# Kernel optimization log

Measured on AMD Instinct MI355X. Metric: run time of the kernel, lower is better.

## Reference

```python
import jax, jax.numpy as jnp
import numpy as np

N_PTS = 2_000_000
RESO = 256          # per-axis resolution of the factorized planes
OUT_DIM = 3         # output_coordinate_dim
RANK = 4            # rank per plane component
FEAT_RESO = 64      # resolution of the final feature grid
FEAT_DIM = 32       # feature_dim
INIT_STD = 0.1


def grid_sample_2d(plane, coords):
    """Bilinear sample. plane: [C,H,W]; coords: [N,2] (x,y) in [-1,1].
    align_corners=True, border clamping. Returns [N,C]."""
    C, H, W = plane.shape
    x = jnp.clip((coords[:, 0] + 1.0) * 0.5 * (W - 1), 0.0, W - 1)
    y = jnp.clip((coords[:, 1] + 1.0) * 0.5 * (H - 1), 0.0, H - 1)
    x0 = jnp.clip(jnp.floor(x), 0, W - 2).astype(jnp.int32)
    y0 = jnp.clip(jnp.floor(y), 0, H - 2).astype(jnp.int32)
    wx = (x - x0)[None, :]
    wy = (y - y0)[None, :]
    v00 = plane[:, y0, x0]
    v01 = plane[:, y0, x0 + 1]
    v10 = plane[:, y0 + 1, x0]
    v11 = plane[:, y0 + 1, x0 + 1]
    out = (v00 * (1 - wx) * (1 - wy) + v01 * wx * (1 - wy)
           + v10 * (1 - wx) * wy + v11 * wx * wy)  # [C,N]
    return out.T


def grid_sample_3d(vol, coords):
    """Trilinear sample. vol: [C,D,H,W]; coords: [N,3] (x,y,z) in [-1,1]
    mapping to (W,H,D). align_corners=True, border clamping. Returns [N,C]."""
    C, D, H, W = vol.shape
    x = jnp.clip((coords[:, 0] + 1.0) * 0.5 * (W - 1), 0.0, W - 1)
    y = jnp.clip((coords[:, 1] + 1.0) * 0.5 * (H - 1), 0.0, H - 1)
    z = jnp.clip((coords[:, 2] + 1.0) * 0.5 * (D - 1), 0.0, D - 1)
    x0 = jnp.clip(jnp.floor(x), 0, W - 2).astype(jnp.int32)
    y0 = jnp.clip(jnp.floor(y), 0, H - 2).astype(jnp.int32)
    z0 = jnp.clip(jnp.floor(z), 0, D - 2).astype(jnp.int32)
    wx = (x - x0)[None, :]
    wy = (y - y0)[None, :]
    wz = (z - z0)[None, :]
    out = jnp.zeros((C, x.shape[0]), dtype=vol.dtype)
    for dz, fz in ((z0, 1 - wz), (z0 + 1, wz)):
        for dy, fy in ((y0, 1 - wy), (y0 + 1, wy)):
            for dx, fx in ((x0, 1 - wx), (x0 + 1, wx)):
                out = out + vol[:, dz, dy, dx] * (fz * fy * fx)
    return out.T


def setup_inputs() -> dict:
    key = jax.random.key(0)
    ks = jax.random.split(key, 5)
    pts = jax.random.uniform(ks[0], (N_PTS, 3), dtype=jnp.float32,
                             minval=-1.0, maxval=1.0)
    C = OUT_DIM * RANK
    plane01 = jax.random.normal(ks[1], (C, RESO, RESO), dtype=jnp.float32) * INIT_STD
    plane02 = jax.random.normal(ks[2], (C, RESO, RESO), dtype=jnp.float32) * INIT_STD
    plane12 = jax.random.normal(ks[3], (C, RESO, RESO), dtype=jnp.float32) * INIT_STD
    features = jax.random.normal(
        ks[4], (FEAT_DIM, FEAT_RESO, FEAT_RESO, FEAT_RESO), dtype=jnp.float32) * INIT_STD
    return {"pts": pts, "plane01": plane01, "plane02": plane02,
            "plane12": plane12, "features": features}


def reference(pts, plane01, plane02, plane12, features):
    # coo_combs = [(0,1),(0,2),(1,2)]; plane ci shaped [out_dim*rank, reso[c1], reso[c0]]
    n = pts.shape[0]
    interp = grid_sample_2d(plane01, pts[:, (0, 1)]).reshape(n, OUT_DIM, RANK)
    interp = interp * grid_sample_2d(plane02, pts[:, (0, 2)]).reshape(n, OUT_DIM, RANK)
    interp = interp * grid_sample_2d(plane12, pts[:, (1, 2)]).reshape(n, OUT_DIM, RANK)
    coords = interp.sum(axis=-1)  # [N, out_dim] -> new coordinates in [-1,1]-ish
    out = grid_sample_3d(features, coords)  # [N, feature_dim]
    return out
```

## Files before the change

kernel.cpp:

```cpp
#include <hip/hip_runtime.h>


constexpr int kNPts   = 2000000;
constexpr int kReso   = 256;
constexpr int kPix    = kReso * kReso;
constexpr int kCPlane = 12;
constexpr int kFReso  = 64;
constexpr int kNVox   = kFReso * kFReso * kFReso;
constexpr int kFDim   = 32;
constexpr int kCellRes = 16;
constexpr int kNCell  = kCellRes * kCellRes * kCellRes;
constexpr int kCap    = 640;
constexpr unsigned kOvCap = 2000000u;

constexpr int kThreads    = 256;
constexpr int kPtsPerScB  = 16384;
constexpr int kScBlocks   = (kNPts + kPtsPerScB - 1) / kPtsPerScB;
constexpr int kPlaneBlocks = (3 * (kPix / 4)) / kThreads;
constexpr int kFeatBlocks  = (kNVox / 4) / kThreads;
constexpr int kPrepBlocks  = kScBlocks + kPlaneBlocks + kFeatBlocks;
constexpr int kOvBlocks    = 16;

constexpr int kStage = 18;
constexpr int kRowF  = kStage * kCPlane;

static __device__ __forceinline__ float clampf(float v, float lo, float hi) {
  return fminf(fmaxf(v, lo), hi);
}

static __device__ __forceinline__ float4 f4_scale_add(float4 v, float s, float4 acc) {
  acc.x = fmaf(v.x, s, acc.x);
  acc.y = fmaf(v.y, s, acc.y);
  acc.z = fmaf(v.z, s, acc.z);
  acc.w = fmaf(v.w, s, acc.w);
  return acc;
}

static __device__ __forceinline__ int cell_of(float x, float y, float z) {
  int xq = min(kCellRes - 1, max(0, (int)((x + 1.0f) * (0.5f * kCellRes))));
  int yq = min(kCellRes - 1, max(0, (int)((y + 1.0f) * (0.5f * kCellRes))));
  int zq = min(kCellRes - 1, max(0, (int)((z + 1.0f) * (0.5f * kCellRes))));
  return (zq * kCellRes + yq) * kCellRes + xq;
}

static __device__ __forceinline__ void sample_plane_tr(
    const float* __restrict__ plane, float cx, float cy, float4 r[3]) {
  float x = clampf((cx + 1.0f) * 0.5f * (float)(kReso - 1), 0.0f, (float)(kReso - 1));
  float y = clampf((cy + 1.0f) * 0.5f * (float)(kReso - 1), 0.0f, (float)(kReso - 1));
  float fx0 = fminf(floorf(x), (float)(kReso - 2));
  float fy0 = fminf(floorf(y), (float)(kReso - 2));
  int x0 = (int)fx0;
  int y0 = (int)fy0;
  float wx = x - fx0;
  float wy = y - fy0;
  float w00 = (1.0f - wx) * (1.0f - wy);
  float w01 = wx * (1.0f - wy);
  float w10 = (1.0f - wx) * wy;
  float w11 = wx * wy;
  const float4* v00 = (const float4*)(plane + (size_t)(y0 * kReso + x0) * kCPlane);
  const float4* v01 = (const float4*)(plane + (size_t)(y0 * kReso + x0 + 1) * kCPlane);
  const float4* v10 = (const float4*)(plane + (size_t)((y0 + 1) * kReso + x0) * kCPlane);
  const float4* v11 = (const float4*)(plane + (size_t)((y0 + 1) * kReso + x0 + 1) * kCPlane);
#pragma unroll
  for (int i = 0; i < 3; ++i) {
    float4 acc = make_float4(0.f, 0.f, 0.f, 0.f);
    acc = f4_scale_add(v00[i], w00, acc);
    acc = f4_scale_add(v01[i], w01, acc);
    acc = f4_scale_add(v10[i], w10, acc);
    acc = f4_scale_add(v11[i], w11, acc);
    r[i] = acc;
  }
}

static __device__ __forceinline__ void bilin_lds(
    const float* __restrict__ sp, int lc, int lr, float wc, float wr, float4 r[3]) {
  const float* t00 = sp + (lr * kStage + lc) * kCPlane;
  const float* t01 = t00 + kCPlane;
  const float* t10 = t00 + kRowF;
  const float* t11 = t10 + kCPlane;
  float w00 = (1.0f - wc) * (1.0f - wr);
  float w01 = wc * (1.0f - wr);
  float w10 = (1.0f - wc) * wr;
  float w11 = wc * wr;
#pragma unroll
  for (int i = 0; i < 3; ++i) {
    float4 acc = make_float4(0.f, 0.f, 0.f, 0.f);
    acc = f4_scale_add(((const float4*)t00)[i], w00, acc);
    acc = f4_scale_add(((const float4*)t01)[i], w01, acc);
    acc = f4_scale_add(((const float4*)t10)[i], w10, acc);
    acc = f4_scale_add(((const float4*)t11)[i], w11, acc);
    r[i] = acc;
  }
}


__global__ __launch_bounds__(256) void prep_fused(
    const float* __restrict__ pts,
    const float* __restrict__ p0, const float* __restrict__ p1,
    const float* __restrict__ p2, const float* __restrict__ featSrc,
    float* __restrict__ planeT, float* __restrict__ featT,
    unsigned* __restrict__ counts, unsigned* __restrict__ ovcnt,
    unsigned* __restrict__ ovlist, unsigned* __restrict__ buckets) {
  __shared__ unsigned short s_cellid[kPtsPerScB];
  __shared__ unsigned s_hist[kNCell];
  __shared__ unsigned s_loc[kNCell];

  int b = blockIdx.x;
  int tid = threadIdx.x;

  if (b < kScBlocks) {
    for (int i = tid; i < kNCell; i += kThreads) s_hist[i] = 0u;
    __syncthreads();

    size_t base = (size_t)b * kPtsPerScB;
#pragma unroll 4
    for (int k = 0; k < kPtsPerScB / kThreads; ++k) {
      int sl = k * kThreads + tid;
      size_t g = base + sl;
      unsigned short cid = 0xFFFFu;
      if (g < (size_t)kNPts) {
        const float* pp = pts + 3 * g;
        cid = (unsigned short)cell_of(pp[0], pp[1], pp[2]);
        atomicAdd(&s_hist[cid], 1u);
      }
      s_cellid[sl] = cid;
    }
    __syncthreads();

    for (int c = tid; c < kNCell; c += kThreads) {
      unsigned h = s_hist[c];
      s_loc[c] = 0u;
      s_hist[c] = h ? atomicAdd(&counts[c], h) : 0u;
    }
    __syncthreads();

#pragma unroll 4
    for (int k = 0; k < kPtsPerScB / kThreads; ++k) {
      int sl = k * kThreads + tid;
      unsigned short cid = s_cellid[sl];
      if (cid == 0xFFFFu) continue;
      unsigned r = atomicAdd(&s_loc[cid], 1u);
      unsigned pos = s_hist[cid] + r;
      unsigned idx = (unsigned)(base + sl);
      if (pos < (unsigned)kCap) {
        buckets[(size_t)cid * kCap + pos] = idx;
      } else {
        unsigned op = atomicAdd(ovcnt, 1u);
        if (op < kOvCap) ovlist[op] = idx;
      }
    }
  } else if (b < kScBlocks + kPlaneBlocks) {
    int t = (b - kScBlocks) * kThreads + tid;
    constexpr int quarter = kPix / 4;
    int p = t / quarter;
    int pix4 = (t % quarter) * 4;
    const float* src = (p == 0) ? p0 : (p == 1) ? p1 : p2;
    float4 v[kCPlane];
#pragma unroll
    for (int c = 0; c < kCPlane; ++c)
      v[c] = *(const float4*)(src + (size_t)c * kPix + pix4);
    float* dstb = planeT + ((size_t)p * kPix + pix4) * kCPlane;
#pragma unroll
    for (int j = 0; j < 4; ++j) {
      float e[kCPlane];
#pragma unroll
      for (int c = 0; c < kCPlane; ++c) {
        const float* vc = (const float*)&v[c];
        e[c] = vc[j];
      }
      float4* dst = (float4*)(dstb + (size_t)j * kCPlane);
      dst[0] = make_float4(e[0], e[1], e[2], e[3]);
      dst[1] = make_float4(e[4], e[5], e[6], e[7]);
      dst[2] = make_float4(e[8], e[9], e[10], e[11]);
    }
  } else {
    int t = (b - kScBlocks - kPlaneBlocks) * kThreads + tid;
    int vox4 = t * 4;
#pragma unroll
    for (int chunk = 0; chunk < 4; ++chunk) {
      float4 v[8];
#pragma unroll
      for (int c8 = 0; c8 < 8; ++c8) {
        int c = chunk * 8 + c8;
        v[c8] = *(const float4*)(featSrc + (size_t)c * kNVox + vox4);
      }
#pragma unroll
      for (int j = 0; j < 4; ++j) {
        float e[8];
#pragma unroll
        for (int c8 = 0; c8 < 8; ++c8) e[c8] = ((const float*)&v[c8])[j];
        float4* dst = (float4*)(featT + (size_t)(vox4 + j) * kFDim + chunk * 8);
        dst[0] = make_float4(e[0], e[1], e[2], e[3]);
        dst[1] = make_float4(e[4], e[5], e[6], e[7]);
      }
    }
  }
}


__global__ __launch_bounds__(256) void lrh_cells(
    const float* __restrict__ pts, const float* __restrict__ planeT,
    const float* __restrict__ feat,
    const unsigned* __restrict__ counts, const unsigned* __restrict__ buckets,
    const unsigned* __restrict__ ovcnt, const unsigned* __restrict__ ovlist,
    float* __restrict__ out) {
  __shared__ float s_plane[3][kStage * kRowF];

  int b = blockIdx.x;
  int tid = threadIdx.x;

  if (b < kNCell) {
    int cellx = b & (kCellRes - 1);
    int celly = (b >> 4) & (kCellRes - 1);
    int cellz = b >> 8;
    int sx = min(cellx * 255 / 16, kReso - kStage);
    int sy = min(celly * 255 / 16, kReso - kStage);
    int sz = min(cellz * 255 / 16, kReso - kStage);
    const int colS[3] = {sx, sx, sy};
    const int rowS[3] = {sy, sz, sz};

#pragma unroll
    for (int p = 0; p < 3; ++p) {
      const float* src = planeT + (size_t)p * kPix * kCPlane;
      float* dst = s_plane[p];
      for (int i = tid; i < kStage * (kRowF / 4); i += kThreads) {
        int r = i / (kRowF / 4);
        int q = i - r * (kRowF / 4);
        float4 v = *(const float4*)(src +
            ((size_t)(rowS[p] + r) * kReso + colS[p]) * kCPlane + q * 4);
        *(float4*)(dst + r * kRowF + q * 4) = v;
      }
    }
    __syncthreads();

    unsigned craw = counts[b];
    int cnt = craw < (unsigned)kCap ? (int)craw : kCap;

    for (int base = 0; base < cnt; base += kThreads) {
      int slot = base + tid;
      if (slot >= cnt) break;
      int n = (int)buckets[(size_t)b * kCap + slot];

      const float* pp = pts + 3 * (size_t)n;
      float xx = pp[0], yy = pp[1], zz = pp[2];

      float px = clampf((xx + 1.0f) * 0.5f * (float)(kReso - 1), 0.0f, (float)(kReso - 1));
      float py = clampf((yy + 1.0f) * 0.5f * (float)(kReso - 1), 0.0f, (float)(kReso - 1));
      float pz = clampf((zz + 1.0f) * 0.5f * (float)(kReso - 1), 0.0f, (float)(kReso - 1));
      float fx0 = fminf(floorf(px), (float)(kReso - 2));
      float fy0 = fminf(floorf(py), (float)(kReso - 2));
      float fz0 = fminf(floorf(pz), (float)(kReso - 2));
      float wx = px - fx0, wy = py - fy0, wz = pz - fz0;
      int lx = min(max((int)fx0 - sx, 0), kStage - 2);
      int ly = min(max((int)fy0 - sy, 0), kStage - 2);
      int lz = min(max((int)fz0 - sz, 0), kStage - 2);

      float4 a[3], bb[3], c3[3];
      bilin_lds(s_plane[0], lx, ly, wx, wy, a);
      bilin_lds(s_plane[1], lx, lz, wx, wz, bb);
      bilin_lds(s_plane[2], ly, lz, wy, wz, c3);

      float coord[3];
#pragma unroll
      for (int d = 0; d < 3; ++d) {
        float mx = a[d].x * bb[d].x * c3[d].x;
        float my = a[d].y * bb[d].y * c3[d].y;
        float mz = a[d].z * bb[d].z * c3[d].z;
        float mw = a[d].w * bb[d].w * c3[d].w;
        coord[d] = (mx + my) + (mz + mw);
      }

      float gx = clampf((coord[0] + 1.0f) * 0.5f * (float)(kFReso - 1), 0.0f, (float)(kFReso - 1));
      float gy = clampf((coord[1] + 1.0f) * 0.5f * (float)(kFReso - 1), 0.0f, (float)(kFReso - 1));
      float gz = clampf((coord[2] + 1.0f) * 0.5f * (float)(kFReso - 1), 0.0f, (float)(kFReso - 1));
      float gfx0 = fminf(floorf(gx), (float)(kFReso - 2));
      float gfy0 = fminf(floorf(gy), (float)(kFReso - 2));
      float gfz0 = fminf(floorf(gz), (float)(kFReso - 2));
      int ix0 = (int)gfx0;
      int iy0 = (int)gfy0;
      int iz0 = (int)gfz0;
      float fwx = gx - gfx0, fwy = gy - gfy0, fwz = gz - gfz0;

      float acc[kFDim];
#pragma unroll
      for (int c = 0; c < kFDim; ++c) acc[c] = 0.0f;

#pragma unroll
      for (int dz = 0; dz < 2; ++dz) {
        float fzw = dz ? fwz : (1.0f - fwz);
#pragma unroll
        for (int dy = 0; dy < 2; ++dy) {
          float fyw = dy ? fwy : (1.0f - fwy);
#pragma unroll
          for (int dx = 0; dx < 2; ++dx) {
            float w = fzw * fyw * (dx ? fwx : (1.0f - fwx));
            int vox = ((iz0 + dz) * kFReso + (iy0 + dy)) * kFReso + (ix0 + dx);
            const float4* v = (const float4*)(feat + (size_t)vox * kFDim);
#pragma unroll
            for (int k = 0; k < 8; ++k) {
              float4 t = v[k];
              acc[4 * k + 0] = fmaf(t.x, w, acc[4 * k + 0]);
              acc[4 * k + 1] = fmaf(t.y, w, acc[4 * k + 1]);
              acc[4 * k + 2] = fmaf(t.z, w, acc[4 * k + 2]);
              acc[4 * k + 3] = fmaf(t.w, w, acc[4 * k + 3]);
            }
          }
        }
      }

      float4* o = (float4*)(out + (size_t)n * kFDim);
#pragma unroll
      for (int k = 0; k < 8; ++k)
        o[k] = make_float4(acc[4 * k], acc[4 * k + 1], acc[4 * k + 2], acc[4 * k + 3]);
    }
  } else {
    unsigned ov = *ovcnt;
    if (ov > kOvCap) ov = kOvCap;
    const float* p01 = planeT;
    const float* p02 = planeT + (size_t)kPix * kCPlane;
    const float* p12 = planeT + (size_t)2 * kPix * kCPlane;
    for (unsigned i = (unsigned)(b - kNCell) * kThreads + tid; i < ov;
         i += (unsigned)kOvBlocks * kThreads) {
      int n = (int)ovlist[i];
      float cx = pts[3 * (size_t)n + 0];
      float cy = pts[3 * (size_t)n + 1];
      float cz = pts[3 * (size_t)n + 2];

      float4 a[3], bb[3], c3[3];
      sample_plane_tr(p01, cx, cy, a);
      sample_plane_tr(p02, cx, cz, bb);
      sample_plane_tr(p12, cy, cz, c3);

      float coord[3];
#pragma unroll
      for (int d = 0; d < 3; ++d) {
        float mx = a[d].x * bb[d].x * c3[d].x;
        float my = a[d].y * bb[d].y * c3[d].y;
        float mz = a[d].z * bb[d].z * c3[d].z;
        float mw = a[d].w * bb[d].w * c3[d].w;
        coord[d] = (mx + my) + (mz + mw);
      }

      float gx = clampf((coord[0] + 1.0f) * 0.5f * (float)(kFReso - 1), 0.0f, (float)(kFReso - 1));
      float gy = clampf((coord[1] + 1.0f) * 0.5f * (float)(kFReso - 1), 0.0f, (float)(kFReso - 1));
      float gz = clampf((coord[2] + 1.0f) * 0.5f * (float)(kFReso - 1), 0.0f, (float)(kFReso - 1));
      float fx0 = fminf(floorf(gx), (float)(kFReso - 2));
      float fy0 = fminf(floorf(gy), (float)(kFReso - 2));
      float fz0 = fminf(floorf(gz), (float)(kFReso - 2));
      int ix0 = (int)fx0;
      int iy0 = (int)fy0;
      int iz0 = (int)fz0;
      float wx = gx - fx0, wy = gy - fy0, wz = gz - fz0;

      float acc[kFDim];
#pragma unroll
      for (int c = 0; c < kFDim; ++c) acc[c] = 0.0f;
#pragma unroll
      for (int dz = 0; dz < 2; ++dz) {
        float fzw = dz ? wz : (1.0f - wz);
#pragma unroll
        for (int dy = 0; dy < 2; ++dy) {
          float fyw = dy ? wy : (1.0f - wy);
#pragma unroll
          for (int dx = 0; dx < 2; ++dx) {
            float w = fzw * fyw * (dx ? wx : (1.0f - wx));
            int vox = ((iz0 + dz) * kFReso + (iy0 + dy)) * kFReso + (ix0 + dx);
            const float4* v = (const float4*)(feat + (size_t)vox * kFDim);
#pragma unroll
            for (int k = 0; k < 8; ++k) {
              float4 t = v[k];
              acc[4 * k + 0] = fmaf(t.x, w, acc[4 * k + 0]);
              acc[4 * k + 1] = fmaf(t.y, w, acc[4 * k + 1]);
              acc[4 * k + 2] = fmaf(t.z, w, acc[4 * k + 2]);
              acc[4 * k + 3] = fmaf(t.w, w, acc[4 * k + 3]);
            }
          }
        }
      }
      float4* o = (float4*)(out + (size_t)n * kFDim);
#pragma unroll
      for (int k = 0; k < 8; ++k)
        o[k] = make_float4(acc[4 * k], acc[4 * k + 1], acc[4 * k + 2], acc[4 * k + 3]);
    }
  }
}

extern "C" void kernel_launch(void* const* d_in, const int* in_sizes, int n_in,
                              void* d_out, int out_size, void* d_ws, size_t ws_size,
                              hipStream_t stream) {
  const float* pts  = (const float*)d_in[0];
  const float* p01  = (const float*)d_in[1];
  const float* p02  = (const float*)d_in[2];
  const float* p12  = (const float*)d_in[3];
  const float* feat = (const float*)d_in[4];
  float* out = (float*)d_out;

  const size_t off_planeT  = 0;
  const size_t sz_planeT   = (size_t)3 * kPix * kCPlane * sizeof(float);
  const size_t off_featT   = off_planeT + sz_planeT;
  const size_t sz_featT    = (size_t)kNVox * kFDim * sizeof(float);
  const size_t off_counts  = off_featT + sz_featT;
  const size_t sz_counts   = (size_t)kNCell * sizeof(unsigned);
  const size_t off_ovcnt   = off_counts + sz_counts;
  const size_t sz_ovcnt    = 256;
  const size_t off_ovlist  = off_ovcnt + sz_ovcnt;
  const size_t sz_ovlist   = (size_t)kOvCap * sizeof(unsigned);
  const size_t off_buckets = off_ovlist + sz_ovlist;
  const size_t sz_buckets  = (size_t)kNCell * kCap * sizeof(unsigned);
  const size_t need = off_buckets + sz_buckets;

  if (ws_size < need) return;

  char* wsb = (char*)d_ws;
  float*    planeT  = (float*)(wsb + off_planeT);
  float*    featT   = (float*)(wsb + off_featT);
  unsigned* counts  = (unsigned*)(wsb + off_counts);
  unsigned* ovcnt   = (unsigned*)(wsb + off_ovcnt);
  unsigned* ovlist  = (unsigned*)(wsb + off_ovlist);
  unsigned* buckets = (unsigned*)(wsb + off_buckets);

  hipMemsetAsync(counts, 0, sz_counts + sz_ovcnt, stream);
  hipLaunchKernelGGL(prep_fused, dim3(kPrepBlocks), dim3(kThreads), 0, stream,
                     pts, p01, p02, p12, feat, planeT, featT,
                     counts, ovcnt, ovlist, buckets);
  hipLaunchKernelGGL(lrh_cells, dim3(kNCell + kOvBlocks), dim3(kThreads), 0, stream,
                     pts, planeT, featT, counts, buckets, ovcnt, ovlist, out);
}
```

Baseline: 526.3 us.

## Split trilinear feature gather across 8 lanes per point and widen prep blocks

```diff
diff --git a/kernel.cpp b/kernel.cpp
--- a/kernel.cpp
+++ b/kernel.cpp
@@ -13,11 +13,12 @@
 constexpr int kCap    = 640;
 constexpr unsigned kOvCap = 2000000u;
 
-constexpr int kThreads    = 256;
-constexpr int kPtsPerScB  = 16384;
-constexpr int kScBlocks   = (kNPts + kPtsPerScB - 1) / kPtsPerScB;
-constexpr int kPlaneBlocks = (3 * (kPix / 4)) / kThreads;
-constexpr int kFeatBlocks  = (kNVox / 4) / kThreads;
+constexpr int kThreads     = 256;
+constexpr int kPrepThreads = 1024;
+constexpr int kPtsPerScB   = 16384;
+constexpr int kScBlocks    = (kNPts + kPtsPerScB - 1) / kPtsPerScB;
+constexpr int kPlaneBlocks = (3 * (kPix / 4)) / kPrepThreads;
+constexpr int kFeatBlocks  = (kNVox / 4) / kPrepThreads;
 constexpr int kPrepBlocks  = kScBlocks + kPlaneBlocks + kFeatBlocks;
 constexpr int kOvBlocks    = 16;
 
@@ -94,7 +95,7 @@
 }
 
 
-__global__ __launch_bounds__(256) void prep_fused(
+__global__ __launch_bounds__(1024) void prep_fused(
     const float* __restrict__ pts,
     const float* __restrict__ p0, const float* __restrict__ p1,
     const float* __restrict__ p2, const float* __restrict__ featSrc,
@@ -109,13 +110,12 @@
   int tid = threadIdx.x;
 
   if (b < kScBlocks) {
-    for (int i = tid; i < kNCell; i += kThreads) s_hist[i] = 0u;
+    for (int i = tid; i < kNCell; i += kPrepThreads) s_hist[i] = 0u;
     __syncthreads();
 
     size_t base = (size_t)b * kPtsPerScB;
-#pragma unroll 4
-    for (int k = 0; k < kPtsPerScB / kThreads; ++k) {
-      int sl = k * kThreads + tid;
+    for (int k = 0; k < kPtsPerScB / kPrepThreads; ++k) {
+      int sl = k * kPrepThreads + tid;
       size_t g = base + sl;
       unsigned short cid = 0xFFFFu;
       if (g < (size_t)kNPts) {
@@ -127,16 +127,15 @@
     }
     __syncthreads();
 
-    for (int c = tid; c < kNCell; c += kThreads) {
+    for (int c = tid; c < kNCell; c += kPrepThreads) {
       unsigned h = s_hist[c];
       s_loc[c] = 0u;
       s_hist[c] = h ? atomicAdd(&counts[c], h) : 0u;
     }
     __syncthreads();
 
-#pragma unroll 4
-    for (int k = 0; k < kPtsPerScB / kThreads; ++k) {
-      int sl = k * kThreads + tid;
+    for (int k = 0; k < kPtsPerScB / kPrepThreads; ++k) {
+      int sl = k * kPrepThreads + tid;
       unsigned short cid = s_cellid[sl];
       if (cid == 0xFFFFu) continue;
       unsigned r = atomicAdd(&s_loc[cid], 1u);
@@ -150,7 +149,7 @@
       }
     }
   } else if (b < kScBlocks + kPlaneBlocks) {
-    int t = (b - kScBlocks) * kThreads + tid;
+    int t = (b - kScBlocks) * kPrepThreads + tid;
     constexpr int quarter = kPix / 4;
     int p = t / quarter;
     int pix4 = (t % quarter) * 4;
@@ -174,7 +173,7 @@
       dst[2] = make_float4(e[8], e[9], e[10], e[11]);
     }
   } else {
-    int t = (b - kScBlocks - kPlaneBlocks) * kThreads + tid;
+    int t = (b - kScBlocks - kPlaneBlocks) * kPrepThreads + tid;
     int vox4 = t * 4;
 #pragma unroll
     for (int chunk = 0; chunk < 4; ++chunk) {
@@ -205,6 +204,11 @@
     const unsigned* __restrict__ ovcnt, const unsigned* __restrict__ ovlist,
     float* __restrict__ out) {
   __shared__ float s_plane[3][kStage * kRowF];
+  __shared__ int   s_n[kThreads];
+  __shared__ int   s_vox[kThreads];
+  __shared__ float s_wx[kThreads];
+  __shared__ float s_wy[kThreads];
+  __shared__ float s_wz[kThreads];
 
   int b = blockIdx.x;
   int tid = threadIdx.x;
@@ -238,80 +242,100 @@
 
     for (int base = 0; base < cnt; base += kThreads) {
       int slot = base + tid;
-      if (slot >= cnt) break;
-      int n = (int)buckets[(size_t)b * kCap + slot];
-
-      const float* pp = pts + 3 * (size_t)n;
-      float xx = pp[0], yy = pp[1], zz = pp[2];
-
-      float px = clampf((xx + 1.0f) * 0.5f * (float)(kReso - 1), 0.0f, (float)(kReso - 1));
-      float py = clampf((yy + 1.0f) * 0.5f * (float)(kReso - 1), 0.0f, (float)(kReso - 1));
-      float pz = clampf((zz + 1.0f) * 0.5f * (float)(kReso - 1), 0.0f, (float)(kReso - 1));
-      float fx0 = fminf(floorf(px), (float)(kReso - 2));
-      float fy0 = fminf(floorf(py), (float)(kReso - 2));
-      float fz0 = fminf(floorf(pz), (float)(kReso - 2));
-      float wx = px - fx0, wy = py - fy0, wz = pz - fz0;
-      int lx = min(max((int)fx0 - sx, 0), kStage - 2);
-      int ly = min(max((int)fy0 - sy, 0), kStage - 2);
-      int lz = min(max((int)fz0 - sz, 0), kStage - 2);
-
-      float4 a[3], bb[3], c3[3];
-      bilin_lds(s_plane[0], lx, ly, wx, wy, a);
-      bilin_lds(s_plane[1], lx, lz, wx, wz, bb);
-      bilin_lds(s_plane[2], ly, lz, wy, wz, c3);
-
-      float coord[3];
-#pragma unroll
-      for (int d = 0; d < 3; ++d) {
-        float mx = a[d].x * bb[d].x * c3[d].x;
-        float my = a[d].y * bb[d].y * c3[d].y;
-        float mz = a[d].z * bb[d].z * c3[d].z;
-        float mw = a[d].w * bb[d].w * c3[d].w;
-        coord[d] = (mx + my) + (mz + mw);
-      }
-
-      float gx = clampf((coord[0] + 1.0f) * 0.5f * (float)(kFReso - 1), 0.0f, (float)(kFReso - 1));
-      float gy = clampf((coord[1] + 1.0f) * 0.5f * (float)(kFReso - 1), 0.0f, (float)(kFReso - 1));
-      float gz = clampf((coord[2] + 1.0f) * 0.5f * (float)(kFReso - 1), 0.0f, (float)(kFReso - 1));
-      float gfx0 = fminf(floorf(gx), (float)(kFReso - 2));
-      float gfy0 = fminf(floorf(gy), (float)(kFReso - 2));
-      float gfz0 = fminf(floorf(gz), (float)(kFReso - 2));
-      int ix0 = (int)gfx0;
-      int iy0 = (int)gfy0;
-      int iz0 = (int)gfz0;
-      float fwx = gx - gfx0, fwy = gy - gfy0, fwz = gz - gfz0;
-
-      float acc[kFDim];
-#pragma unroll
-      for (int c = 0; c < kFDim; ++c) acc[c] = 0.0f;
-
-#pragma unroll
-      for (int dz = 0; dz < 2; ++dz) {
-        float fzw = dz ? fwz : (1.0f - fwz);
-#pragma unroll
-        for (int dy = 0; dy < 2; ++dy) {
-          float fyw = dy ? fwy : (1.0f - fwy);
-#pragma unroll
-          for (int dx = 0; dx < 2; ++dx) {
-            float w = fzw * fyw * (dx ? fwx : (1.0f - fwx));
-            int vox = ((iz0 + dz) * kFReso + (iy0 + dy)) * kFReso + (ix0 + dx);
-            const float4* v = (const float4*)(feat + (size_t)vox * kFDim);
-#pragma unroll
-            for (int k = 0; k < 8; ++k) {
-              float4 t = v[k];
-              acc[4 * k + 0] = fmaf(t.x, w, acc[4 * k + 0]);
-              acc[4 * k + 1] = fmaf(t.y, w, acc[4 * k + 1]);
-              acc[4 * k + 2] = fmaf(t.z, w, acc[4 * k + 2]);
-              acc[4 * k + 3] = fmaf(t.w, w, acc[4 * k + 3]);
-            }
-          }
+      int n = -1;
+      int ivox = 0;
+      float wxo = 0.f, wyo = 0.f, wzo = 0.f;
+      if (slot < cnt) {
+        n = (int)buckets[(size_t)b * kCap + slot];
+        const float* pp = pts + 3 * (size_t)n;
+        float xx = pp[0], yy = pp[1], zz = pp[2];
+
+        float px = clampf((xx + 1.0f) * 0.5f * (float)(kReso - 1), 0.0f, (float)(kReso - 1));
+        float py = clampf((yy + 1.0f) * 0.5f * (float)(kReso - 1), 0.0f, (float)(kReso - 1));
+        float pz = clampf((zz + 1.0f) * 0.5f * (float)(kReso - 1), 0.0f, (float)(kReso - 1));
+        float fx0 = fminf(floorf(px), (float)(kReso - 2));
+        float fy0 = fminf(floorf(py), (float)(kReso - 2));
+        float fz0 = fminf(floorf(pz), (float)(kReso - 2));
+        float wx = px - fx0, wy = py - fy0, wz = pz - fz0;
+        int lx = min(max((int)fx0 - sx, 0), kStage - 2);
+        int ly = min(max((int)fy0 - sy, 0), kStage - 2);
+        int lz = min(max((int)fz0 - sz, 0), kStage - 2);
+
+        float4 a[3], bb[3], c3[3];
+        bilin_lds(s_plane[0], lx, ly, wx, wy, a);
+        bilin_lds(s_plane[1], lx, lz, wx, wz, bb);
+        bilin_lds(s_plane[2], ly, lz, wy, wz, c3);
+
+        float coord[3];
+#pragma unroll
+        for (int d = 0; d < 3; ++d) {
+          float mx = a[d].x * bb[d].x * c3[d].x;
+          float my = a[d].y * bb[d].y * c3[d].y;
+          float mz = a[d].z * bb[d].z * c3[d].z;
+          float mw = a[d].w * bb[d].w * c3[d].w;
+          coord[d] = (mx + my) + (mz + mw);
         }
-      }
-
-      float4* o = (float4*)(out + (size_t)n * kFDim);
-#pragma unroll
-      for (int k = 0; k < 8; ++k)
-        o[k] = make_float4(acc[4 * k], acc[4 * k + 1], acc[4 * k + 2], acc[4 * k + 3]);
+
+        float gx = clampf((coord[0] + 1.0f) * 0.5f * (float)(kFReso - 1), 0.0f, (float)(kFReso - 1));
+        float gy = clampf((coord[1] + 1.0f) * 0.5f * (float)(kFReso - 1), 0.0f, (float)(kFReso - 1));
+        float gz = clampf((coord[2] + 1.0f) * 0.5f * (float)(kFReso - 1), 0.0f, (float)(kFReso - 1));
+        float gfx0 = fminf(floorf(gx), (float)(kFReso - 2));
+        float gfy0 = fminf(floorf(gy), (float)(kFReso - 2));
+        float gfz0 = fminf(floorf(gz), (float)(kFReso - 2));
+        int ix0 = (int)gfx0;
+        int iy0 = (int)gfy0;
+        int iz0 = (int)gfz0;
+        wxo = gx - gfx0;
+        wyo = gy - gfy0;
+        wzo = gz - gfz0;
+        ivox = (iz0 * kFReso + iy0) * kFReso + ix0;
+      }
+      s_n[tid] = n;
+      s_vox[tid] = ivox;
+      s_wx[tid] = wxo;
+      s_wy[tid] = wyo;
+      s_wz[tid] = wzo;
+      __syncthreads();
+
+      int l4 = (tid & 7) * 4;
+      int oct = tid >> 3;
+      for (int step = 0; step < 8; ++step) {
+        int s = step * 32 + oct;
+        int n2 = s_n[s];
+        if (n2 < 0) continue;
+        int vox = s_vox[s];
+        float wx2 = s_wx[s], wy2 = s_wy[s], wz2 = s_wz[s];
+        float ux = 1.0f - wx2, uy = 1.0f - wy2, uz = 1.0f - wz2;
+
+        const float* fb = feat + (size_t)vox * kFDim + l4;
+        float4 t0 = *(const float4*)(fb);
+        float4 t1 = *(const float4*)(fb + kFDim);
+        float4 t2 = *(const float4*)(fb + kFReso * kFDim);
+        float4 t3 = *(const float4*)(fb + kFReso * kFDim + kFDim);
+        float4 t4 = *(const float4*)(fb + kFReso * kFReso * kFDim);
+        float4 t5 = *(const float4*)(fb + kFReso * kFReso * kFDim + kFDim);
+        float4 t6 = *(const float4*)(fb + kFReso * kFReso * kFDim + kFReso * kFDim);
+        float4 t7 = *(const float4*)(fb + kFReso * kFReso * kFDim + kFReso * kFDim + kFDim);
+
+        float a0 = uz * uy, a1 = uz * wy2, a2 = wz2 * uy, a3 = wz2 * wy2;
+        float w0 = a0 * ux, w1 = a0 * wx2;
+        float w2 = a1 * ux, w3 = a1 * wx2;
+        float w4 = a2 * ux, w5 = a2 * wx2;
+        float w6 = a3 * ux, w7 = a3 * wx2;
+
+        float4 acc;
+        acc.x = t0.x * w0; acc.y = t0.y * w0; acc.z = t0.z * w0; acc.w = t0.w * w0;
+        acc = f4_scale_add(t1, w1, acc);
+        acc = f4_scale_add(t2, w2, acc);
+        acc = f4_scale_add(t3, w3, acc);
+        acc = f4_scale_add(t4, w4, acc);
+        acc = f4_scale_add(t5, w5, acc);
+        acc = f4_scale_add(t6, w6, acc);
+        acc = f4_scale_add(t7, w7, acc);
+
+        *(float4*)(out + (size_t)n2 * kFDim + l4) = acc;
+      }
+      __syncthreads();
     }
   } else {
     unsigned ov = *ovcnt;
@@ -420,7 +444,7 @@
   unsigned* buckets = (unsigned*)(wsb + off_buckets);
 
   hipMemsetAsync(counts, 0, sz_counts + sz_ovcnt, stream);
-  hipLaunchKernelGGL(prep_fused, dim3(kPrepBlocks), dim3(kThreads), 0, stream,
+  hipLaunchKernelGGL(prep_fused, dim3(kPrepBlocks), dim3(kPrepThreads), 0, stream,
                      pts, p01, p02, p12, feat, planeT, featT,
                      counts, ovcnt, ovlist, buckets);
   hipLaunchKernelGGL(lrh_cells, dim3(kNCell + kOvBlocks), dim3(kThreads), 0, stream,
```

Measured after the change: 489.0 us. 7.1% less time.
